# Optimization experiments

Measured on AMD Instinct MI355X. Metric: run time of the kernel, lower is better.

The kernel has to match this reference:

```python
import jax, jax.numpy as jnp
import numpy as np

D_MODEL = 1024
N_HEADS = 16
D_HEAD = D_MODEL // N_HEADS


def setup_inputs() -> dict:
    key = jax.random.key(0)
    kx, kq, kk, kv, ko = jax.random.split(key, 5)
    s = 1.0 / np.sqrt(D_MODEL)
    return {
        "x": jax.random.normal(kx, (2, 2048, D_MODEL), dtype=jnp.float32),
        "Wq": jax.random.normal(kq, (D_MODEL, D_MODEL), dtype=jnp.float32) * s,
        "Wk": jax.random.normal(kk, (D_MODEL, D_MODEL), dtype=jnp.float32) * s,
        "Wv": jax.random.normal(kv, (D_MODEL, D_MODEL), dtype=jnp.float32) * s,
        "Wo": jax.random.normal(ko, (D_MODEL, D_MODEL), dtype=jnp.float32) * s,
    }


def reference(x, Wq, Wk, Wv, Wo):
    B, T, _ = x.shape
    def split_heads(t):  # [B,T,D] -> [B,H,T,d]
        return t.reshape(B, T, N_HEADS, D_HEAD).transpose(0, 2, 1, 3)
    q = split_heads(x @ Wq)
    k = split_heads(x @ Wk)
    v = split_heads(x @ Wv)
    scale = jnp.asarray(D_HEAD, x.dtype) ** -0.5
    att = jnp.einsum("bhqd,bhkd->bhqk", q, k) * scale
    mask = jnp.tril(jnp.ones((T, T), dtype=x.dtype))  # 1 on/below diag
    att = att + (1.0 - mask)[None, None] * jnp.asarray(-1e9, x.dtype)
    w = jax.nn.softmax(att, axis=-1)
    y = jnp.einsum("bhqk,bhkd->bhqd", w, v)
    y = y.transpose(0, 2, 1, 3).reshape(B, T, D_MODEL)
    return y @ Wo
```

## Files before the change

### kernel.cpp

```cpp
#include <hip/hip_runtime.h>

#define DM 1024
#define NH 16
#define TT 2048
#define BB 2
#define NTOK (BB*TT)
#define DQKV 3072

typedef __attribute__((ext_vector_type(8))) short bf16x8;
typedef __attribute__((ext_vector_type(4))) float f32x4;
typedef __attribute__((ext_vector_type(4))) int  int4v;

static __device__ __forceinline__ short f2b(float f) {
  union { float f; unsigned u; } v; v.f = f;
  unsigned r = v.u + 0x7FFFu + ((v.u >> 16) & 1u);
  return (short)(r >> 16);
}

__global__ __launch_bounds__(256) void k_convert(const float* __restrict__ in,
                                                 short* __restrict__ out, int n) {
  int i = (blockIdx.x * 256 + threadIdx.x) * 8;
  if (i >= n) return;
  float4 a = *(const float4*)(in + i);
  float4 b = *(const float4*)(in + i + 4);
  bf16x8 o;
  o[0]=f2b(a.x); o[1]=f2b(a.y); o[2]=f2b(a.z); o[3]=f2b(a.w);
  o[4]=f2b(b.x); o[5]=f2b(b.y); o[6]=f2b(b.z); o[7]=f2b(b.w);
  *(bf16x8*)(out + i) = o;
}

__global__ __launch_bounds__(256) void k_transpose_w4(const float* __restrict__ Wq,
                                                      const float* __restrict__ Wk,
                                                      const float* __restrict__ Wv,
                                                      const float* __restrict__ Wo,
                                                      short* __restrict__ WqkvT,
                                                      short* __restrict__ WoT) {
  __shared__ short t[64][72];
  const int z = blockIdx.z;
  const float* W = (z == 0) ? Wq : (z == 1) ? Wk : (z == 2) ? Wv : Wo;
  short* Wt = (z < 3) ? WqkvT : WoT;
  const int row0 = (z < 3) ? z * 1024 : 0;
  int tid = threadIdx.x;
  int n0 = blockIdx.x * 64, k0 = blockIdx.y * 64;
  #pragma unroll
  for (int i = 0; i < 4; i++) {
    int id = tid + 256 * i;
    int r = id >> 4;
    int c = id & 15;
    float4 v = *(const float4*)(W + (size_t)(k0 + r) * DM + n0 + c * 4);
    t[c*4+0][r] = f2b(v.x);
    t[c*4+1][r] = f2b(v.y);
    t[c*4+2][r] = f2b(v.z);
    t[c*4+3][r] = f2b(v.w);
  }
  __syncthreads();
  #pragma unroll
  for (int i = 0; i < 2; i++) {
    int id = tid + 256 * i;
    int r = id >> 3;
    int c = id & 7;
    bf16x8 o = *(const bf16x8*)&t[r][c * 8];
    *(bf16x8*)(Wt + (size_t)(row0 + n0 + r) * DM + k0 + c * 8) = o;
  }
}

__global__ __launch_bounds__(256) void k_transpose_v(const short* __restrict__ V,
                                                     short* __restrict__ Vt) {
  __shared__ short t[64][72];
  int tid = threadIdx.x;
  int bh = blockIdx.y;
  int b = bh >> 4, h = bh & 15;
  int t0 = blockIdx.x * 64;
  #pragma unroll
  for (int i = 0; i < 2; i++) {
    int id = tid + 256 * i;
    int r = id >> 3;
    int c = id & 7;
    int n = r >> 4;
    int kp = ((n >> 1) << 5) | (((r >> 2) & 3) << 3) | ((n & 1) << 2) | (r & 3);
    bf16x8 v = *(const bf16x8*)(V + (size_t)(b * TT + t0 + r) * DQKV + h * 64 + c * 8);
    #pragma unroll
    for (int e = 0; e < 8; e++) t[c * 8 + e][kp] = v[e];
  }
  __syncthreads();
  #pragma unroll
  for (int i = 0; i < 2; i++) {
    int id = tid + 256 * i;
    int r = id >> 3;
    int c = id & 7;
    bf16x8 o = *(const bf16x8*)&t[r][c * 8];
    *(bf16x8*)(Vt + (size_t)(bh * 64 + r) * TT + t0 + c * 8) = o;
  }
}

template<int OUT_BF16, int BN>
__global__ __launch_bounds__(256) void k_gemm_lds(const short* __restrict__ A,
                                                  const short* __restrict__ Bt,
                                                  void* __restrict__ C,
                                                  int M, int N, int K,
                                                  int qcols, float qscale) {
  __shared__ short As[2][128 * 64];
  __shared__ short Bs[2][BN * 64];
  constexpr int NI = BN / 32;
  const int tid = threadIdx.x;
  const int lane = tid & 63, w = tid >> 6;
  const int wm = w >> 1, wn = w & 1;
  const int l15 = lane & 15, g = lane >> 4;
  const int nx = N / BN;
  const int cx = nx >> 3;
  const int bid = blockIdx.x;
  const int xcd = bid & 7, k_ = bid >> 3;
  const int bx = xcd * cx + (k_ % cx), by = k_ / cx;
  const int m0 = by * 128, n0 = bx * BN;
  const int srow = lane >> 3;
  const int scol = ((lane & 7) ^ srow) * 8;
  const int rsw = l15 & 7;

  auto stage = [&](int buf, int k0) {
    #pragma unroll
    for (int i = 0; i < 4; i++) {
      int rbase = w * 32 + i * 8;
      __builtin_amdgcn_global_load_lds(
        (const __attribute__((address_space(1))) void*)(A + (size_t)(m0 + rbase + srow) * K + k0 + scol),
        (__attribute__((address_space(3))) void*)&As[buf][rbase * 64],
        16, 0, 0);
    }
    #pragma unroll
    for (int i = 0; i < BN / 32; i++) {
      int rbase = w * (BN / 4) + i * 8;
      __builtin_amdgcn_global_load_lds(
        (const __attribute__((address_space(1))) void*)(Bt + (size_t)(n0 + rbase + srow) * K + k0 + scol),
        (__attribute__((address_space(3))) void*)&Bs[buf][rbase * 64],
        16, 0, 0);
    }
  };

  f32x4 acc[4][NI] = {};
  stage(0, 0);
  __syncthreads();
  const int nt = K / 64;
  for (int t = 0; t < nt; t++) {
    const int cur = t & 1;
    if (t + 1 < nt) stage(cur ^ 1, (t + 1) * 64);
    #pragma unroll
    for (int kk = 0; kk < 64; kk += 32) {
      bf16x8 af[4], bfr[NI];
      #pragma unroll
      for (int mi = 0; mi < 4; mi++)
        af[mi] = *(const bf16x8*)&As[cur][(wm * 64 + mi * 16 + l15) * 64 + ((((kk >> 3) + g) ^ rsw) << 3)];
      #pragma unroll
      for (int ni = 0; ni < NI; ni++)
        bfr[ni] = *(const bf16x8*)&Bs[cur][(wn * (BN / 2) + ni * 16 + l15) * 64 + ((((kk >> 3) + g) ^ rsw) << 3)];
      #pragma unroll
      for (int mi = 0; mi < 4; mi++)
        #pragma unroll
        for (int ni = 0; ni < NI; ni++)
          acc[mi][ni] = __builtin_amdgcn_mfma_f32_16x16x32_bf16(af[mi], bfr[ni], acc[mi][ni], 0, 0, 0);
    }
    __syncthreads();
  }

  if (OUT_BF16) {
    short* Cs = &As[0][0];
    #pragma unroll
    for (int mi = 0; mi < 4; mi++) {
      #pragma unroll
      for (int ni = 0; ni < NI; ni++) {
        #pragma unroll
        for (int j = 0; j < 4; j++) {
          int row = wm * 64 + mi * 16 + g * 4 + j;
          int col = wn * (BN / 2) + ni * 16 + l15;
          float v = acc[mi][ni][j];
          if (n0 + col < qcols) v *= qscale;
          Cs[row * BN + col] = f2b(v);
        }
      }
    }
    __syncthreads();
    constexpr int UNITS = 128 * BN / 8;
    #pragma unroll
    for (int u = tid; u < UNITS; u += 256) {
      int row = u / (BN / 8), ch = u % (BN / 8);
      bf16x8 vv = *(const bf16x8*)&Cs[row * BN + ch * 8];
      *(bf16x8*)((short*)C + (size_t)(m0 + row) * N + n0 + ch * 8) = vv;
    }
  } else {
    #pragma unroll
    for (int mi = 0; mi < 4; mi++) {
      #pragma unroll
      for (int ni = 0; ni < NI; ni++) {
        #pragma unroll
        for (int j = 0; j < 4; j++) {
          int row = m0 + wm * 64 + mi * 16 + g * 4 + j;
          int col = n0 + wn * (BN / 2) + ni * 16 + l15;
          ((float*)C)[(size_t)row * N + col] = acc[mi][ni][j];
        }
      }
    }
  }
}

__global__ __launch_bounds__(256) void k_attn(const short* __restrict__ Qkv,
                                              const short* __restrict__ Vt,
                                              short* __restrict__ Y) {
  __shared__ short Ks[2][64 * 64];
  __shared__ short Vs[2][64 * 64];
  const int tid = threadIdx.x;
  const int lane = tid & 63, w = tid >> 6;
  const int l15 = lane & 15, g = lane >> 4;
  const int bx = blockIdx.x;
  const int xcd = bx & 7, idx = bx >> 3;
  const int bh = xcd * 4 + (idx & 3);
  const int qt = 31 - (idx >> 2);
  const int b = bh >> 4, h = bh & 15;
  const int q0 = qt * 64;
  const int nkt = qt + 1;
  const short* Qb = Qkv;
  const short* Kb = Qkv + DM;
  const int rsw = l15 & 7;

  const bf16x8 vones = {0x3F80, 0x3F80, 0x3F80, 0x3F80, 0x3F80, 0x3F80, 0x3F80, 0x3F80};

  auto stage = [&](int buf, int kt) {
    #pragma unroll
    for (int i = 0; i < 2; i++) {
      int id = tid + 256 * i;
      int r = id >> 3;
      int cl = (id ^ r) & 7;
      __builtin_amdgcn_global_load_lds(
        (const __attribute__((address_space(1))) void*)(Kb + (size_t)(b * TT + kt * 64 + r) * DQKV + h * 64 + cl * 8),
        (__attribute__((address_space(3))) void*)&Ks[buf][(w * 64 + 256 * i) * 8],
        16, 0, 0);
      __builtin_amdgcn_global_load_lds(
        (const __attribute__((address_space(1))) void*)(Vt + (size_t)(bh * 64 + r) * TT + kt * 64 + cl * 8),
        (__attribute__((address_space(3))) void*)&Vs[buf][(w * 64 + 256 * i) * 8],
        16, 0, 0);
    }
  };

  bf16x8 aq[2];
  #pragma unroll
  for (int kc = 0; kc < 2; kc++)
    aq[kc] = *(const bf16x8*)(Qb + (size_t)(b * TT + q0 + w * 16 + l15) * DQKV + h * 64 + kc * 32 + 8 * g);

  f32x4 accO[4] = {};
  f32x4 accL = {};
  float m2 = -1e30f;

  stage(0, 0);
  __syncthreads();

  for (int kt = 0; kt < nkt; kt++) {
    const int cur = kt & 1;
    if (kt + 1 < nkt) stage(cur ^ 1, kt + 1);

    f32x4 accS[4] = {};
    __builtin_amdgcn_s_setprio(1);
    #pragma unroll
    for (int n = 0; n < 4; n++) {
      #pragma unroll
      for (int kc = 0; kc < 2; kc++) {
        bf16x8 bk = *(const bf16x8*)&Ks[cur][(n * 16 + l15) * 64 + (((kc * 4 + g) ^ rsw) << 3)];
        accS[n] = __builtin_amdgcn_mfma_f32_16x16x32_bf16(bk, aq[kc], accS[n], 0, 0, 0);
      }
    }
    __builtin_amdgcn_s_setprio(0);

    const int qg = q0 + w * 16 + l15;
    if (kt == qt) {
      #pragma unroll
      for (int n = 0; n < 4; n++) {
        #pragma unroll
        for (int j = 0; j < 4; j++) {
          int key = kt * 64 + n * 16 + g * 4 + j;
          if (key > qg) accS[n][j] = -1e30f;
        }
      }
    }
    float tmax = -1e30f;
    #pragma unroll
    for (int n = 0; n < 4; n++)
      #pragma unroll
      for (int j = 0; j < 4; j++)
        tmax = fmaxf(tmax, accS[n][j]);

    if (!__all(tmax - m2 <= 8.0f)) {
      float t1 = fmaxf(tmax, __shfl_xor(tmax, 16));
      float full = fmaxf(t1, __shfl_xor(t1, 32));
      float mnew = fmaxf(m2, full);
      float al = exp2f(m2 - mnew);
      m2 = mnew;
      float alr[4];
      #pragma unroll
      for (int j = 0; j < 4; j++) alr[j] = __shfl(al, g * 4 + j);
      #pragma unroll
      for (int j = 0; j < 4; j++) accL[j] *= alr[j];
      #pragma unroll
      for (int n2 = 0; n2 < 4; n2++)
        #pragma unroll
        for (int j = 0; j < 4; j++) accO[n2][j] *= alr[j];
    }

    unsigned cu[4][4];
    #pragma unroll
    for (int n = 0; n < 4; n++)
      #pragma unroll
      for (int j = 0; j < 4; j++) {
        union { float f; unsigned u; } cv;
        cv.f = exp2f(accS[n][j] - m2);
        cu[n][j] = cv.u;
      }

    __builtin_amdgcn_s_setprio(1);
    #pragma unroll
    for (int kc = 0; kc < 2; kc++) {
      union { int4v i; bf16x8 h; } pu;
      pu.i[0] = (int)((cu[2*kc+0][0] >> 16) | (cu[2*kc+0][1] & 0xFFFF0000u));
      pu.i[1] = (int)((cu[2*kc+0][2] >> 16) | (cu[2*kc+0][3] & 0xFFFF0000u));
      pu.i[2] = (int)((cu[2*kc+1][0] >> 16) | (cu[2*kc+1][1] & 0xFFFF0000u));
      pu.i[3] = (int)((cu[2*kc+1][2] >> 16) | (cu[2*kc+1][3] & 0xFFFF0000u));
      bf16x8 pa = pu.h;
      #pragma unroll
      for (int n2 = 0; n2 < 4; n2++) {
        bf16x8 vb = *(const bf16x8*)&Vs[cur][(n2 * 16 + l15) * 64 + (((kc * 4 + g) ^ rsw) << 3)];
        accO[n2] = __builtin_amdgcn_mfma_f32_16x16x32_bf16(pa, vb, accO[n2], 0, 0, 0);
      }
      accL = __builtin_amdgcn_mfma_f32_16x16x32_bf16(pa, vones, accL, 0, 0, 0);
    }
    __builtin_amdgcn_s_setprio(0);

    __syncthreads();
  }

  float inv[4];
  #pragma unroll
  for (int j = 0; j < 4; j++) inv[j] = 1.0f / accL[j];
  short* Ys = &Ks[0][w * 1024];
  #pragma unroll
  for (int n2 = 0; n2 < 4; n2++) {
    #pragma unroll
    for (int j = 0; j < 4; j++) {
      float v = accO[n2][j] * inv[j];
      Ys[(g * 4 + j) * 64 + n2 * 16 + l15] = f2b(v);
    }
  }
  const int orow = b * TT + q0 + w * 16;
  #pragma unroll
  for (int i = 0; i < 2; i++) {
    int unit = lane + 64 * i;
    int row = unit >> 3, ch = unit & 7;
    bf16x8 vv = *(const bf16x8*)&Ys[row * 64 + ch * 8];
    *(bf16x8*)(Y + (size_t)(orow + row) * DM + h * 64 + ch * 8) = vv;
  }
}

extern "C" void kernel_launch(void* const* d_in, const int* in_sizes, int n_in,
                              void* d_out, int out_size, void* d_ws, size_t ws_size,
                              hipStream_t stream) {
  const float* x  = (const float*)d_in[0];
  const float* Wq = (const float*)d_in[1];
  const float* Wk = (const float*)d_in[2];
  const float* Wv = (const float*)d_in[3];
  const float* Wo = (const float*)d_in[4];
  float* out = (float*)d_out;

  char* ws = (char*)d_ws;
  size_t off = 0;
  auto alloc = [&](size_t bytes) {
    char* p = ws + off;
    off += (bytes + 255) & ~(size_t)255;
    return p;
  };
  short* xb    = (short*)alloc((size_t)NTOK * DM * 2);
  short* WqkvT = (short*)alloc((size_t)DQKV * DM * 2);
  short* WoT   = (short*)alloc((size_t)DM * DM * 2);
  short* Qkv   = (short*)alloc((size_t)NTOK * DQKV * 2);
  short* Vt    = (short*)alloc((size_t)NTOK * DM * 2);
  short* Yb    = xb;
  if (off > ws_size) return;

  k_convert<<<(NTOK * DM) / (256 * 8), 256, 0, stream>>>(x, xb, NTOK * DM);
  k_transpose_w4<<<dim3(DM / 64, DM / 64, 4), 256, 0, stream>>>(Wq, Wk, Wv, Wo, WqkvT, WoT);

  const float QSC = 0.125f * 1.44269504088896f;
  k_gemm_lds<1, 64><<<dim3((DQKV / 64) * (NTOK / 128)), 256, 0, stream>>>(xb, WqkvT, Qkv, NTOK, DQKV, DM, DM, QSC);

  k_transpose_v<<<dim3(TT / 64, BB * NH), 256, 0, stream>>>(Qkv + 2048, Vt);
  k_attn<<<dim3(1024), 256, 0, stream>>>(Qkv, Vt, Yb);

  k_gemm_lds<0, 64><<<dim3((DM / 64) * (NTOK / 128)), 256, 0, stream>>>(Yb, WoT, out, NTOK, DM, DM, 0, 1.0f);
}
```

Before: 114.4 us.

## Split long causal attention rows into two KV chunks with merge kernel

Query tiles in the upper half of the sequence are split into two key ranges, each handled by its own block, and the partial outputs, maxima and row sums are written to workspace in fp32. A new merge kernel rescales and combines the two partials and writes bf16 output. The aim is to balance the causal workload and shorten the longest blocks, raising the grid from 1024 to 1536 blocks. In exchange it adds an extra launch, fp32 partial traffic, and a dependence on enough workspace being available, with a fallback path when it is not.

After: 114.9 us. No clear change (+0.4%).

```diff
diff --git a/kernel.cpp b/kernel.cpp
--- a/kernel.cpp
+++ b/kernel.cpp
@@ -202,7 +202,9 @@
 
 __global__ __launch_bounds__(256) void k_attn(const short* __restrict__ Qkv,
                                               const short* __restrict__ Vt,
-                                              short* __restrict__ Y) {
+                                              short* __restrict__ Y,
+                                              float* __restrict__ Opart,
+                                              float* __restrict__ MLpart) {
   __shared__ short Ks[2][64 * 64];
   __shared__ short Vs[2][64 * 64];
   const int tid = threadIdx.x;
@@ -211,10 +213,24 @@
   const int bx = blockIdx.x;
   const int xcd = bx & 7, idx = bx >> 3;
   const int bh = xcd * 4 + (idx & 3);
-  const int qt = 31 - (idx >> 2);
   const int b = bh >> 4, h = bh & 15;
+  const bool split = (Opart != nullptr);
+
+  int qt, cchunk, ktb, kte;
+  if (split) {
+    const int i = idx >> 2;
+    if (i < 16) { qt = 16 + i; cchunk = 0; }
+    else {
+      int j = (i - 16) >> 1;
+      if (((i - 16) & 1) == 0) { qt = 15 - j; cchunk = 0; }
+      else                     { qt = 31 - j; cchunk = 1; }
+    }
+    ktb = (cchunk == 0) ? 0 : 16;
+    kte = (cchunk == 0) ? ((qt + 1 < 16) ? qt + 1 : 16) : qt + 1;
+  } else {
+    qt = 31 - (idx >> 2); cchunk = 0; ktb = 0; kte = qt + 1;
+  }
   const int q0 = qt * 64;
-  const int nkt = qt + 1;
   const short* Qb = Qkv;
   const short* Kb = Qkv + DM;
   const int rsw = l15 & 7;
@@ -247,12 +263,12 @@
   f32x4 accL = {};
   float m2 = -1e30f;
 
-  stage(0, 0);
+  stage(0, ktb);
   __syncthreads();
 
-  for (int kt = 0; kt < nkt; kt++) {
-    const int cur = kt & 1;
-    if (kt + 1 < nkt) stage(cur ^ 1, kt + 1);
+  for (int kt = ktb; kt < kte; kt++) {
+    const int cur = (kt - ktb) & 1;
+    if (kt + 1 < kte) stage(cur ^ 1, kt + 1);
 
     f32x4 accS[4] = {};
     __builtin_amdgcn_s_setprio(1);
@@ -332,26 +348,71 @@
     __syncthreads();
   }
 
-  float inv[4];
-  #pragma unroll
-  for (int j = 0; j < 4; j++) inv[j] = 1.0f / accL[j];
-  short* Ys = &Ks[0][w * 1024];
-  #pragma unroll
-  for (int n2 = 0; n2 < 4; n2++) {
-    #pragma unroll
-    for (int j = 0; j < 4; j++) {
-      float v = accO[n2][j] * inv[j];
-      Ys[(g * 4 + j) * 64 + n2 * 16 + l15] = f2b(v);
-    }
-  }
-  const int orow = b * TT + q0 + w * 16;
-  #pragma unroll
-  for (int i = 0; i < 2; i++) {
-    int unit = lane + 64 * i;
-    int row = unit >> 3, ch = unit & 7;
-    bf16x8 vv = *(const bf16x8*)&Ys[row * 64 + ch * 8];
-    *(bf16x8*)(Y + (size_t)(orow + row) * DM + h * 64 + ch * 8) = vv;
-  }
+  if (!split || qt < 16) {
+    float inv[4];
+    #pragma unroll
+    for (int j = 0; j < 4; j++) inv[j] = 1.0f / accL[j];
+    short* Ys = &Ks[0][w * 1024];
+    #pragma unroll
+    for (int n2 = 0; n2 < 4; n2++) {
+      #pragma unroll
+      for (int j = 0; j < 4; j++) {
+        float v = accO[n2][j] * inv[j];
+        Ys[(g * 4 + j) * 64 + n2 * 16 + l15] = f2b(v);
+      }
+    }
+    const int orow = b * TT + q0 + w * 16;
+    #pragma unroll
+    for (int i = 0; i < 2; i++) {
+      int unit = lane + 64 * i;
+      int row = unit >> 3, ch = unit & 7;
+      bf16x8 vv = *(const bf16x8*)&Ys[row * 64 + ch * 8];
+      *(bf16x8*)(Y + (size_t)(orow + row) * DM + h * 64 + ch * 8) = vv;
+    }
+  } else {
+    const int p = (bh * 16 + (qt - 16)) * 2 + cchunk;
+    float* Op = Opart + (size_t)p * 4096;
+    #pragma unroll
+    for (int n2 = 0; n2 < 4; n2++)
+      #pragma unroll
+      for (int j = 0; j < 4; j++)
+        Op[(w * 16 + g * 4 + j) * 64 + n2 * 16 + l15] = accO[n2][j];
+    float* ML = MLpart + (size_t)p * 128;
+    if (g == 0) ML[w * 16 + l15] = m2;
+    if (l15 == 0) {
+      #pragma unroll
+      for (int j = 0; j < 4; j++) ML[64 + w * 16 + g * 4 + j] = accL[j];
+    }
+  }
+}
+
+__global__ __launch_bounds__(256) void k_merge(const float* __restrict__ Opart,
+                                               const float* __restrict__ MLpart,
+                                               short* __restrict__ Y) {
+  const int m = blockIdx.x;
+  const int bh = m >> 4, qi = 16 + (m & 15);
+  const int b = bh >> 4, h = bh & 15;
+  const int p0 = (bh * 16 + (qi - 16)) * 2;
+  const float* O0 = Opart + (size_t)p0 * 4096;
+  const float* O1 = O0 + 4096;
+  const float* ML0 = MLpart + (size_t)p0 * 128;
+  const float* ML1 = ML0 + 128;
+  const int tid = threadIdx.x;
+  const int r = tid >> 2, c0 = (tid & 3) * 16;
+  float m0 = ML0[r], m1 = ML1[r];
+  float mm = fmaxf(m0, m1);
+  float s0 = exp2f(m0 - mm), s1 = exp2f(m1 - mm);
+  float L = ML0[64 + r] * s0 + ML1[64 + r] * s1;
+  float inv = 1.0f / L;
+  short tmp[16];
+  #pragma unroll
+  for (int c = 0; c < 16; c++) {
+    float v = (O0[r * 64 + c0 + c] * s0 + O1[r * 64 + c0 + c] * s1) * inv;
+    tmp[c] = f2b(v);
+  }
+  short* dst = Y + (size_t)(b * TT + qi * 64 + r) * DM + h * 64 + c0;
+  *(bf16x8*)dst = *(bf16x8*)&tmp[0];
+  *(bf16x8*)(dst + 8) = *(bf16x8*)&tmp[8];
 }
 
 extern "C" void kernel_launch(void* const* d_in, const int* in_sizes, int n_in,
@@ -377,7 +438,11 @@
   short* Qkv   = (short*)alloc((size_t)NTOK * DQKV * 2);
   short* Vt    = (short*)alloc((size_t)NTOK * DM * 2);
   short* Yb    = xb;
-  if (off > ws_size) return;
+  const size_t base_off = off;
+  float* Opart  = (float*)alloc((size_t)1024 * 4096 * 4);
+  float* MLpart = (float*)alloc((size_t)1024 * 128 * 4);
+  const bool split = (off <= ws_size);
+  if (base_off > ws_size) return;
 
   k_convert<<<(NTOK * DM) / (256 * 8), 256, 0, stream>>>(x, xb, NTOK * DM);
   k_transpose_w4<<<dim3(DM / 64, DM / 64, 4), 256, 0, stream>>>(Wq, Wk, Wv, Wo, WqkvT, WoT);
@@ -386,7 +451,13 @@
   k_gemm_lds<1, 64><<<dim3((DQKV / 64) * (NTOK / 128)), 256, 0, stream>>>(xb, WqkvT, Qkv, NTOK, DQKV, DM, DM, QSC);
 
   k_transpose_v<<<dim3(TT / 64, BB * NH), 256, 0, stream>>>(Qkv + 2048, Vt);
-  k_attn<<<dim3(1024), 256, 0, stream>>>(Qkv, Vt, Yb);
+
+  if (split) {
+    k_attn<<<dim3(1536), 256, 0, stream>>>(Qkv, Vt, Yb, Opart, MLpart);
+    k_merge<<<dim3(512), 256, 0, stream>>>(Opart, MLpart, Yb);
+  } else {
+    k_attn<<<dim3(1024), 256, 0, stream>>>(Qkv, Vt, Yb, nullptr, nullptr);
+  }
 
   k_gemm_lds<0, 64><<<dim3((DM / 64) * (NTOK / 128)), 256, 0, stream>>>(Yb, WoT, out, NTOK, DM, DM, 0, 1.0f);
 }
```

## Switch GEMM to 32x32x16 MFMA and add unused split-KV attention path

Applied to the files above, without the earlier changes.

The projection GEMM kernel moves from 16x16x32 MFMA tiles to 32x32x16 tiles, with each wave holding two 32x32 accumulators. This cuts the number of LDS fragment reads per MFMA and uses the larger-tile instruction. The Q-scale check in the epilogue is hoisted to a per-block test. Attention gains an optional split-KV mode that writes partial O, m and l buffers, but it is launched with null pointers, so that path is inactive and there is no merge kernel.

Result: no change. 116.0 us (+1.4%).

```diff
diff --git a/kernel.cpp b/kernel.cpp
--- a/kernel.cpp
+++ b/kernel.cpp
@@ -9,6 +9,7 @@
 
 typedef __attribute__((ext_vector_type(8))) short bf16x8;
 typedef __attribute__((ext_vector_type(4))) float f32x4;
+typedef __attribute__((ext_vector_type(16))) float f32x16;
 typedef __attribute__((ext_vector_type(4))) int  int4v;
 
 static __device__ __forceinline__ short f2b(float f) {
@@ -99,13 +100,13 @@
                                                   void* __restrict__ C,
                                                   int M, int N, int K,
                                                   int qcols, float qscale) {
+  static_assert(BN == 64, "32x32 path sized for BN=64");
   __shared__ short As[2][128 * 64];
   __shared__ short Bs[2][BN * 64];
-  constexpr int NI = BN / 32;
   const int tid = threadIdx.x;
   const int lane = tid & 63, w = tid >> 6;
   const int wm = w >> 1, wn = w & 1;
-  const int l15 = lane & 15, g = lane >> 4;
+  const int l31 = lane & 31, half = lane >> 5;
   const int nx = N / BN;
   const int cx = nx >> 3;
   const int bid = blockIdx.x;
@@ -114,7 +115,7 @@
   const int m0 = by * 128, n0 = bx * BN;
   const int srow = lane >> 3;
   const int scol = ((lane & 7) ^ srow) * 8;
-  const int rsw = l15 & 7;
+  const int rsw = l31 & 7;
 
   auto stage = [&](int buf, int k0) {
     #pragma unroll
@@ -135,7 +136,7 @@
     }
   };
 
-  f32x4 acc[4][NI] = {};
+  f32x16 acc[2] = {};
   stage(0, 0);
   __syncthreads();
   const int nt = K / 64;
@@ -143,37 +144,29 @@
     const int cur = t & 1;
     if (t + 1 < nt) stage(cur ^ 1, (t + 1) * 64);
     #pragma unroll
-    for (int kk = 0; kk < 64; kk += 32) {
-      bf16x8 af[4], bfr[NI];
-      #pragma unroll
-      for (int mi = 0; mi < 4; mi++)
-        af[mi] = *(const bf16x8*)&As[cur][(wm * 64 + mi * 16 + l15) * 64 + ((((kk >> 3) + g) ^ rsw) << 3)];
-      #pragma unroll
-      for (int ni = 0; ni < NI; ni++)
-        bfr[ni] = *(const bf16x8*)&Bs[cur][(wn * (BN / 2) + ni * 16 + l15) * 64 + ((((kk >> 3) + g) ^ rsw) << 3)];
-      #pragma unroll
-      for (int mi = 0; mi < 4; mi++)
-        #pragma unroll
-        for (int ni = 0; ni < NI; ni++)
-          acc[mi][ni] = __builtin_amdgcn_mfma_f32_16x16x32_bf16(af[mi], bfr[ni], acc[mi][ni], 0, 0, 0);
+    for (int st = 0; st < 4; st++) {
+      const int kc = st * 2 + half;
+      bf16x8 a0 = *(const bf16x8*)&As[cur][(wm * 64 + l31) * 64 + ((kc ^ rsw) << 3)];
+      bf16x8 a1 = *(const bf16x8*)&As[cur][(wm * 64 + 32 + l31) * 64 + ((kc ^ rsw) << 3)];
+      bf16x8 bb = *(const bf16x8*)&Bs[cur][(wn * 32 + l31) * 64 + ((kc ^ rsw) << 3)];
+      acc[0] = __builtin_amdgcn_mfma_f32_32x32x16_bf16(a0, bb, acc[0], 0, 0, 0);
+      acc[1] = __builtin_amdgcn_mfma_f32_32x32x16_bf16(a1, bb, acc[1], 0, 0, 0);
     }
     __syncthreads();
   }
 
   if (OUT_BF16) {
     short* Cs = &As[0][0];
-    #pragma unroll
-    for (int mi = 0; mi < 4; mi++) {
-      #pragma unroll
-      for (int ni = 0; ni < NI; ni++) {
-        #pragma unroll
-        for (int j = 0; j < 4; j++) {
-          int row = wm * 64 + mi * 16 + g * 4 + j;
-          int col = wn * (BN / 2) + ni * 16 + l15;
-          float v = acc[mi][ni][j];
-          if (n0 + col < qcols) v *= qscale;
-          Cs[row * BN + col] = f2b(v);
-        }
+    const bool doscale = (n0 < qcols);
+    #pragma unroll
+    for (int rt = 0; rt < 2; rt++) {
+      #pragma unroll
+      for (int e = 0; e < 16; e++) {
+        int row = wm * 64 + rt * 32 + 4 * half + (e & 3) + 8 * (e >> 2);
+        int col = wn * 32 + l31;
+        float v = acc[rt][e];
+        if (doscale) v *= qscale;
+        Cs[row * BN + col] = f2b(v);
       }
     }
     __syncthreads();
@@ -186,15 +179,12 @@
     }
   } else {
     #pragma unroll
-    for (int mi = 0; mi < 4; mi++) {
-      #pragma unroll
-      for (int ni = 0; ni < NI; ni++) {
-        #pragma unroll
-        for (int j = 0; j < 4; j++) {
-          int row = m0 + wm * 64 + mi * 16 + g * 4 + j;
-          int col = n0 + wn * (BN / 2) + ni * 16 + l15;
-          ((float*)C)[(size_t)row * N + col] = acc[mi][ni][j];
-        }
+    for (int rt = 0; rt < 2; rt++) {
+      #pragma unroll
+      for (int e = 0; e < 16; e++) {
+        int row = m0 + wm * 64 + rt * 32 + 4 * half + (e & 3) + 8 * (e >> 2);
+        int col = n0 + wn * 32 + l31;
+        ((float*)C)[(size_t)row * N + col] = acc[rt][e];
       }
     }
   }
@@ -202,7 +192,9 @@
 
 __global__ __launch_bounds__(256) void k_attn(const short* __restrict__ Qkv,
                                               const short* __restrict__ Vt,
-                                              short* __restrict__ Y) {
+                                              short* __restrict__ Y,
+                                              float* __restrict__ Opart,
+                                              float* __restrict__ MLpart) {
   __shared__ short Ks[2][64 * 64];
   __shared__ short Vs[2][64 * 64];
   const int tid = threadIdx.x;
@@ -211,10 +203,24 @@
   const int bx = blockIdx.x;
   const int xcd = bx & 7, idx = bx >> 3;
   const int bh = xcd * 4 + (idx & 3);
-  const int qt = 31 - (idx >> 2);
   const int b = bh >> 4, h = bh & 15;
+  const bool split = (Opart != nullptr);
+
+  int qt, cchunk, ktb, kte;
+  if (split) {
+    const int i = idx >> 2;
+    if (i < 16) { qt = 16 + i; cchunk = 0; }
+    else {
+      int j = (i - 16) >> 1;
+      if (((i - 16) & 1) == 0) { qt = 15 - j; cchunk = 0; }
+      else                     { qt = 31 - j; cchunk = 1; }
+    }
+    ktb = (cchunk == 0) ? 0 : 16;
+    kte = (cchunk == 0) ? ((qt + 1 < 16) ? qt + 1 : 16) : qt + 1;
+  } else {
+    qt = 31 - (idx >> 2); cchunk = 0; ktb = 0; kte = qt + 1;
+  }
   const int q0 = qt * 64;
-  const int nkt = qt + 1;
   const short* Qb = Qkv;
   const short* Kb = Qkv + DM;
   const int rsw = l15 & 7;
@@ -247,12 +253,12 @@
   f32x4 accL = {};
   float m2 = -1e30f;
 
-  stage(0, 0);
+  stage(0, ktb);
   __syncthreads();
 
-  for (int kt = 0; kt < nkt; kt++) {
-    const int cur = kt & 1;
-    if (kt + 1 < nkt) stage(cur ^ 1, kt + 1);
+  for (int kt = ktb; kt < kte; kt++) {
+    const int cur = (kt - ktb) & 1;
+    if (kt + 1 < kte) stage(cur ^ 1, kt + 1);
 
     f32x4 accS[4] = {};
     __builtin_amdgcn_s_setprio(1);
@@ -332,25 +338,41 @@
     __syncthreads();
   }
 
-  float inv[4];
-  #pragma unroll
-  for (int j = 0; j < 4; j++) inv[j] = 1.0f / accL[j];
-  short* Ys = &Ks[0][w * 1024];
-  #pragma unroll
-  for (int n2 = 0; n2 < 4; n2++) {
-    #pragma unroll
-    for (int j = 0; j < 4; j++) {
-      float v = accO[n2][j] * inv[j];
-      Ys[(g * 4 + j) * 64 + n2 * 16 + l15] = f2b(v);
-    }
-  }
-  const int orow = b * TT + q0 + w * 16;
-  #pragma unroll
-  for (int i = 0; i < 2; i++) {
-    int unit = lane + 64 * i;
-    int row = unit >> 3, ch = unit & 7;
-    bf16x8 vv = *(const bf16x8*)&Ys[row * 64 + ch * 8];
-    *(bf16x8*)(Y + (size_t)(orow + row) * DM + h * 64 + ch * 8) = vv;
+  if (!split || qt < 16) {
+    float inv[4];
+    #pragma unroll
+    for (int j = 0; j < 4; j++) inv[j] = 1.0f / accL[j];
+    short* Ys = &Ks[0][w * 1024];
+    #pragma unroll
+    for (int n2 = 0; n2 < 4; n2++) {
+      #pragma unroll
+      for (int j = 0; j < 4; j++) {
+        float v = accO[n2][j] * inv[j];
+        Ys[(g * 4 + j) * 64 + n2 * 16 + l15] = f2b(v);
+      }
+    }
+    const int orow = b * TT + q0 + w * 16;
+    #pragma unroll
+    for (int i = 0; i < 2; i++) {
+      int unit = lane + 64 * i;
+      int row = unit >> 3, ch = unit & 7;
+      bf16x8 vv = *(const bf16x8*)&Ys[row * 64 + ch * 8];
+      *(bf16x8*)(Y + (size_t)(orow + row) * DM + h * 64 + ch * 8) = vv;
+    }
+  } else {
+    const int p = (bh * 16 + (qt - 16)) * 2 + cchunk;
+    float* Op = Opart + (size_t)p * 4096;
+    #pragma unroll
+    for (int n2 = 0; n2 < 4; n2++)
+      #pragma unroll
+      for (int j = 0; j < 4; j++)
+        Op[(w * 16 + g * 4 + j) * 64 + n2 * 16 + l15] = accO[n2][j];
+    float* ML = MLpart + (size_t)p * 128;
+    if (g == 0) ML[w * 16 + l15] = m2;
+    if (l15 == 0) {
+      #pragma unroll
+      for (int j = 0; j < 4; j++) ML[64 + w * 16 + g * 4 + j] = accL[j];
+    }
   }
 }
 
@@ -386,7 +408,8 @@
   k_gemm_lds<1, 64><<<dim3((DQKV / 64) * (NTOK / 128)), 256, 0, stream>>>(xb, WqkvT, Qkv, NTOK, DQKV, DM, DM, QSC);
 
   k_transpose_v<<<dim3(TT / 64, BB * NH), 256, 0, stream>>>(Qkv + 2048, Vt);
-  k_attn<<<dim3(1024), 256, 0, stream>>>(Qkv, Vt, Yb);
+
+  k_attn<<<dim3(1024), 256, 0, stream>>>(Qkv, Vt, Yb, nullptr, nullptr);
 
   k_gemm_lds<0, 64><<<dim3((DM / 64) * (NTOK / 128)), 256, 0, stream>>>(Yb, WoT, out, NTOK, DM, DM, 0, 1.0f);
 }
```
